# Kernel tuning notes

Hardware: AMD Instinct MI355X
Metric: run time of the kernel (lower is better)

## Reference

```python
import jax, jax.numpy as jnp
import numpy as np

D_MODEL = 1024
NUM_HEADS = 16
DFF = 4096
DEPTH = D_MODEL // NUM_HEADS
EPS = 1e-6


def setup_inputs() -> dict:
    key = jax.random.key(0)
    ks = jax.random.split(key, 12)
    B, S, D = 4, 2048, D_MODEL
    scale = 0.02
    inp = {
        "x": jax.random.normal(ks[0], (B, S, D), dtype=jnp.float32),
        "mask": jnp.zeros((B, 1, 1, S), dtype=jnp.float32),
        "wq": jax.random.normal(ks[1], (D, D), dtype=jnp.float32) * scale,
        "bq": jnp.zeros((D,), dtype=jnp.float32),
        "wk": jax.random.normal(ks[2], (D, D), dtype=jnp.float32) * scale,
        "bk": jnp.zeros((D,), dtype=jnp.float32),
        "wv": jax.random.normal(ks[3], (D, D), dtype=jnp.float32) * scale,
        "bv": jnp.zeros((D,), dtype=jnp.float32),
        "wo": jax.random.normal(ks[4], (D, D), dtype=jnp.float32) * scale,
        "bo": jnp.zeros((D,), dtype=jnp.float32),
        "w1": jax.random.normal(ks[5], (D, DFF), dtype=jnp.float32) * scale,
        "b1": jnp.zeros((DFF,), dtype=jnp.float32),
        "w2": jax.random.normal(ks[6], (DFF, D), dtype=jnp.float32) * scale,
        "b2": jnp.zeros((D,), dtype=jnp.float32),
        "g1": jnp.ones((D,), dtype=jnp.float32),
        "beta1": jnp.zeros((D,), dtype=jnp.float32),
        "g2": jnp.ones((D,), dtype=jnp.float32),
        "beta2": jnp.zeros((D,), dtype=jnp.float32),
    }
    return inp


def _layernorm(x, gamma, beta):
    mu = jnp.mean(x, axis=-1, keepdims=True)
    var = jnp.mean(jnp.square(x - mu), axis=-1, keepdims=True)
    return (x - mu) * jax.lax.rsqrt(var + EPS) * gamma + beta


def _split_heads(t, B, S):
    # [B,S,D] -> [B,H,S,depth]
    return t.reshape(B, S, NUM_HEADS, DEPTH).transpose(0, 2, 1, 3)


def encoder_layer(x, mask, wq, bq, wk, bk, wv, bv, wo, bo,
                  w1, b1, w2, b2, g1, beta1, g2, beta2):
    B, S, D = x.shape
    q = _split_heads(x @ wq + bq, B, S)
    k = _split_heads(x @ wk + bk, B, S)
    v = _split_heads(x @ wv + bv, B, S)
    logits = jnp.einsum("bhqd,bhkd->bhqk", q, k) / jnp.sqrt(
        jnp.asarray(DEPTH, dtype=x.dtype))
    if mask is not None:
        logits = logits + mask * -1e9
    attn = jax.nn.softmax(logits, axis=-1)
    ctx = jnp.einsum("bhqk,bhkd->bhqd", attn, v)
    ctx = ctx.transpose(0, 2, 1, 3).reshape(B, S, D)
    attn_out = ctx @ wo + bo
    out1 = _layernorm(x + attn_out, g1, beta1)
    ffn = jax.nn.relu(out1 @ w1 + b1) @ w2 + b2
    out2 = _layernorm(out1 + ffn, g2, beta2)
    return out2


def reference(x, mask, wq, bq, wk, bk, wv, bv, wo, bo,
              w1, b1, w2, b2, g1, beta1, g2, beta2):
    return encoder_layer(x, mask, wq, bq, wk, bk, wv, bv, wo, bo,
                         w1, b1, w2, b2, g1, beta1, g2, beta2)
```

## Files before the change

kernel.cpp:

```cpp
#include <hip/hip_runtime.h>
#include <cstdint>


#define BATCH 4
#define SEQ   2048
#define DM    1024
#define NH    16
#define DEPTH 64
#define DFF_  4096
#define EPSF  1e-6f

typedef short bf16x8 __attribute__((ext_vector_type(8)));
typedef float f32x4  __attribute__((ext_vector_type(4)));

__device__ __forceinline__ unsigned short f2bf(float f) {
  union { float f; unsigned int u; } v; v.f = f;
  unsigned int u = v.u;
  return (unsigned short)((u + 0x7fffu + ((u >> 16) & 1u)) >> 16);
}

__device__ __forceinline__ void gload_lds16(const void* g, void* l) {
  __builtin_amdgcn_global_load_lds(
      (const __attribute__((address_space(1))) unsigned int*)g,
      (__attribute__((address_space(3))) unsigned int*)l, 16, 0, 0);
}

template<int ACT, int SPLIT, int OUT_BF16>
__global__ __launch_bounds__(256)
void gemm_mfma(const unsigned short* __restrict__ A, const unsigned short* __restrict__ Bt,
               const float* __restrict__ bias, float* __restrict__ Cf,
               unsigned short* __restrict__ Cb, int M, int N, int K)
{
  __shared__ unsigned short As[128 * 32];
  __shared__ unsigned short Bs[128 * 32];
  const int tid  = threadIdx.x;
  const int wid  = tid >> 6;
  const int lane = tid & 63;
  const int wr = wid >> 1, wc = wid & 1;
  const int m0 = blockIdx.y * 128;
  const int n0 = blockIdx.x * 128;

  const int lrow   = lane >> 2;
  const int lchunk = (lane & 3) ^ (lrow & 3);
  const int fr = lane & 15;
  const int kh = lane >> 4;

  f32x4 acc[4][4] = {};

  const char* gA = (const char*)A;
  const char* gB = (const char*)Bt;
  char* lA = (char*)As;
  char* lB = (char*)Bs;

  for (int k0 = 0; k0 < K; k0 += 32) {
#pragma unroll
    for (int seg = 0; seg < 2; ++seg) {
      int r = wid * 32 + seg * 16 + lrow;
      gload_lds16(gA + ((size_t)(m0 + r) * K + k0) * 2 + lchunk * 16,
                  lA + (wid * 32 + seg * 16) * 64);
      gload_lds16(gB + ((size_t)(n0 + r) * K + k0) * 2 + lchunk * 16,
                  lB + (wid * 32 + seg * 16) * 64);
    }
    __syncthreads();
    bf16x8 af[4], bg[4];
#pragma unroll
    for (int i = 0; i < 4; ++i) {
      af[i] = *(const bf16x8*)(lA + (wr * 64 + i * 16 + fr) * 64 + ((kh ^ (fr & 3)) * 16));
      bg[i] = *(const bf16x8*)(lB + (wc * 64 + i * 16 + fr) * 64 + ((kh ^ (fr & 3)) * 16));
    }
#pragma unroll
    for (int i = 0; i < 4; ++i)
#pragma unroll
      for (int j = 0; j < 4; ++j)
        acc[i][j] = __builtin_amdgcn_mfma_f32_16x16x32_bf16(af[i], bg[j], acc[i][j], 0, 0, 0);
    __syncthreads();
  }

  const int rbase = (lane >> 4) * 4;
  const int ccol  = lane & 15;
  float bcol[4];
#pragma unroll
  for (int j = 0; j < 4; ++j) bcol[j] = bias[n0 + wc * 64 + j * 16 + ccol];
#pragma unroll
  for (int i = 0; i < 4; ++i)
#pragma unroll
    for (int jj = 0; jj < 4; ++jj) {
      int row = m0 + wr * 64 + i * 16 + rbase + jj;
#pragma unroll
      for (int j = 0; j < 4; ++j) {
        float vv = acc[i][j][jj] + bcol[j];
        if (ACT) vv = fmaxf(vv, 0.f);
        int col = n0 + wc * 64 + j * 16 + ccol;
        if (SPLIT == 1) {
          int b = row >> 11, s = row & (SEQ - 1);
          int hh = col >> 6, d = col & 63;
          Cb[(((size_t)(b * NH + hh)) * SEQ + s) * DEPTH + d] = f2bf(vv);
        } else if (SPLIT == 2) {
          int b = row >> 11, s = row & (SEQ - 1);
          int hh = col >> 6, d = col & 63;
          Cb[(((size_t)(b * NH + hh)) * DEPTH + d) * SEQ + s] = f2bf(vv);
        } else if (OUT_BF16) {
          Cb[(size_t)row * N + col] = f2bf(vv);
        } else {
          Cf[(size_t)row * N + col] = vv;
        }
      }
    }
}

__global__ __launch_bounds__(256)
void transpose_to_bf16(const float* __restrict__ W, unsigned short* __restrict__ Wt,
                       int K, int N)
{
  __shared__ float t[32][33];
  const int tx = threadIdx.x & 31;
  const int ty = threadIdx.x >> 5;
  const int n0 = blockIdx.x * 32;
  const int k0 = blockIdx.y * 32;
#pragma unroll
  for (int i = 0; i < 4; ++i) {
    int r = ty + i * 8;
    t[r][tx] = W[(size_t)(k0 + r) * N + n0 + tx];
  }
  __syncthreads();
#pragma unroll
  for (int i = 0; i < 4; ++i) {
    int r = ty + i * 8;
    Wt[(size_t)(n0 + r) * K + k0 + tx] = f2bf(t[tx][r]);
  }
}

__global__ __launch_bounds__(256)
void convert_bf16(const float* __restrict__ X, unsigned short* __restrict__ Xb, int n4)
{
  int i = blockIdx.x * 256 + threadIdx.x;
  if (i < n4) {
    float4 v = ((const float4*)X)[i];
    ushort4 r;
    r.x = f2bf(v.x); r.y = f2bf(v.y); r.z = f2bf(v.z); r.w = f2bf(v.w);
    ((ushort4*)Xb)[i] = r;
  }
}

__global__ __launch_bounds__(256)
void attn_mfma(const unsigned short* __restrict__ Qb, const unsigned short* __restrict__ Kb,
               const unsigned short* __restrict__ Vtb, const float* __restrict__ mask,
               unsigned short* __restrict__ ctxb)
{
  __shared__ unsigned short Ks[64 * 64];
  __shared__ unsigned short Vts[64 * 64];
  __shared__ unsigned short Ps[4][16 * 72];
  __shared__ float Ms[SEQ];

  const int tid  = threadIdx.x;
  const int w    = tid >> 6;
  const int lane = tid & 63;
  const int fr   = lane & 15;
  const int kh   = lane >> 4;
  const int rbase = kh * 4;
  const int bh = blockIdx.y;
  const int b  = bh >> 4, hh = bh & 15;
  const int q0 = blockIdx.x * 64;

  for (int i = tid; i < SEQ / 4; i += 256)
    *(float4*)&Ms[i * 4] = *(const float4*)&mask[(size_t)b * SEQ + i * 4];

  const size_t qrow = ((size_t)bh * SEQ + q0 + w * 16 + fr) * DEPTH;
  bf16x8 bq[2];
  bq[0] = *(const bf16x8*)(Qb + qrow + kh * 8);
  bq[1] = *(const bf16x8*)(Qb + qrow + 32 + kh * 8);

  float m_run = -1e30f, l_run = 0.f;
  f32x4 o[4] = {};

  const int stg_chunk = (lane & 7) ^ (lane >> 3);
  const int r8 = lane >> 3;
  unsigned short* Pw = &Ps[w][0];

  for (int kv0 = 0; kv0 < SEQ; kv0 += 64) {
    __syncthreads();
#pragma unroll
    for (int i = 0; i < 2; ++i) {
      int rr = w * 16 + i * 8 + r8;
      gload_lds16((const char*)Kb + (((size_t)bh * SEQ + kv0 + rr) * DEPTH) * 2 + stg_chunk * 16,
                  (char*)Ks + (w * 16 + i * 8) * 128);
      gload_lds16((const char*)Vtb + (((size_t)bh * DEPTH + rr) * SEQ + kv0) * 2 + stg_chunk * 16,
                  (char*)Vts + (w * 16 + i * 8) * 128);
    }
    __syncthreads();

    f32x4 s[4] = {};
#pragma unroll
    for (int ks = 0; ks < 2; ++ks)
#pragma unroll
      for (int j = 0; j < 4; ++j) {
        bf16x8 ak = *(const bf16x8*)((const char*)Ks + (j * 16 + fr) * 128 +
                                     (((ks * 4 + kh) ^ (fr & 7)) * 16));
        s[j] = __builtin_amdgcn_mfma_f32_16x16x32_bf16(ak, bq[ks], s[j], 0, 0, 0);
      }

    float p[16];
    float pmax = -1e30f;
#pragma unroll
    for (int j = 0; j < 4; ++j) {
      float4 mk = *(const float4*)&Ms[kv0 + j * 16 + rbase];
#pragma unroll
      for (int jj = 0; jj < 4; ++jj) {
        float vsc = s[j][jj] * 0.125f + ((const float*)&mk)[jj] * (-1e9f);
        p[j * 4 + jj] = vsc;
        pmax = fmaxf(pmax, vsc);
      }
    }
    pmax = fmaxf(pmax, __shfl_xor(pmax, 16));
    pmax = fmaxf(pmax, __shfl_xor(pmax, 32));
    float mnew = fmaxf(m_run, pmax);
    float sc = __expf(m_run - mnew);
    float rs = 0.f;
#pragma unroll
    for (int t = 0; t < 16; ++t) { p[t] = __expf(p[t] - mnew); rs += p[t]; }
    rs += __shfl_xor(rs, 16);
    rs += __shfl_xor(rs, 32);
    l_run = l_run * sc + rs;
    m_run = mnew;
#pragma unroll
    for (int db = 0; db < 4; ++db) {
      o[db][0] *= sc; o[db][1] *= sc; o[db][2] *= sc; o[db][3] *= sc;
    }

#pragma unroll
    for (int j = 0; j < 4; ++j) {
      unsigned int lo = (unsigned)f2bf(p[j * 4 + 0]) | ((unsigned)f2bf(p[j * 4 + 1]) << 16);
      unsigned int hi = (unsigned)f2bf(p[j * 4 + 2]) | ((unsigned)f2bf(p[j * 4 + 3]) << 16);
      unsigned long long pk = (unsigned long long)lo | ((unsigned long long)hi << 32);
      *(unsigned long long*)((char*)Pw + fr * 144 + (j * 16 + rbase) * 2) = pk;
    }
#pragma unroll
    for (int ks = 0; ks < 2; ++ks) {
      bf16x8 bp = *(const bf16x8*)((char*)Pw + fr * 144 + ks * 64 + kh * 16);
#pragma unroll
      for (int db = 0; db < 4; ++db) {
        bf16x8 av = *(const bf16x8*)((const char*)Vts + (db * 16 + fr) * 128 +
                                     (((ks * 4 + kh) ^ (fr & 7)) * 16));
        o[db] = __builtin_amdgcn_mfma_f32_16x16x32_bf16(av, bp, o[db], 0, 0, 0);
      }
    }
  }

  float inv = 1.f / l_run;
  const int srow = q0 + w * 16 + fr;
#pragma unroll
  for (int db = 0; db < 4; ++db) {
    ushort4 rb;
    rb.x = f2bf(o[db][0] * inv); rb.y = f2bf(o[db][1] * inv);
    rb.z = f2bf(o[db][2] * inv); rb.w = f2bf(o[db][3] * inv);
    *(ushort4*)(ctxb + ((size_t)(b * SEQ + srow)) * DM + hh * 64 + db * 16 + rbase) = rb;
  }
}

template<int DUAL>
__global__ __launch_bounds__(256)
void add_ln_kernel(const float* __restrict__ X, const float* __restrict__ Y,
                   const float* __restrict__ g, const float* __restrict__ be,
                   float* __restrict__ out, unsigned short* __restrict__ outb)
{
  __shared__ float red[8];
  const int row = blockIdx.x;
  const int tid = threadIdx.x;
  const size_t off = (size_t)row * DM + tid * 4;
  float4 xv = *(const float4*)(X + off);
  float4 yv = *(const float4*)(Y + off);
  float v0 = xv.x + yv.x, v1 = xv.y + yv.y, v2 = xv.z + yv.z, v3 = xv.w + yv.w;
  float s = v0 + v1 + v2 + v3;
#pragma unroll
  for (int m = 1; m < 64; m <<= 1) s += __shfl_xor(s, m);
  if ((tid & 63) == 0) red[tid >> 6] = s;
  __syncthreads();
  float mean = (red[0] + red[1] + red[2] + red[3]) * (1.f / DM);
  float d0 = v0 - mean, d1 = v1 - mean, d2 = v2 - mean, d3 = v3 - mean;
  float sq = d0 * d0 + d1 * d1 + d2 * d2 + d3 * d3;
#pragma unroll
  for (int m = 1; m < 64; m <<= 1) sq += __shfl_xor(sq, m);
  if ((tid & 63) == 0) red[4 + (tid >> 6)] = sq;
  __syncthreads();
  float var = (red[4] + red[5] + red[6] + red[7]) * (1.f / DM);
  float inv = rsqrtf(var + EPSF);
  int col = tid * 4;
  float4 r;
  r.x = d0 * inv * g[col + 0] + be[col + 0];
  r.y = d1 * inv * g[col + 1] + be[col + 1];
  r.z = d2 * inv * g[col + 2] + be[col + 2];
  r.w = d3 * inv * g[col + 3] + be[col + 3];
  *(float4*)(out + off) = r;
  if (DUAL) {
    ushort4 rb;
    rb.x = f2bf(r.x); rb.y = f2bf(r.y); rb.z = f2bf(r.z); rb.w = f2bf(r.w);
    *(ushort4*)(outb + off) = rb;
  }
}

extern "C" void kernel_launch(void* const* d_in, const int* in_sizes, int n_in,
                              void* d_out, int out_size, void* d_ws, size_t ws_size,
                              hipStream_t stream)
{
  const float* x    = (const float*)d_in[0];
  const float* mask = (const float*)d_in[1];
  const float* wq   = (const float*)d_in[2];
  const float* bq   = (const float*)d_in[3];
  const float* wk   = (const float*)d_in[4];
  const float* bk   = (const float*)d_in[5];
  const float* wv   = (const float*)d_in[6];
  const float* bv   = (const float*)d_in[7];
  const float* wo   = (const float*)d_in[8];
  const float* bo   = (const float*)d_in[9];
  const float* w1   = (const float*)d_in[10];
  const float* b1   = (const float*)d_in[11];
  const float* w2   = (const float*)d_in[12];
  const float* b2   = (const float*)d_in[13];
  const float* g1   = (const float*)d_in[14];
  const float* be1  = (const float*)d_in[15];
  const float* g2   = (const float*)d_in[16];
  const float* be2  = (const float*)d_in[17];
  float* out = (float*)d_out;
  char* wsb = (char*)d_ws;

  unsigned short* qb   = (unsigned short*)(wsb);
  unsigned short* kb   = (unsigned short*)(wsb + (16u << 20));
  unsigned short* vtb  = (unsigned short*)(wsb + (32u << 20));
  unsigned short* ctxb = (unsigned short*)(wsb + (48u << 20));
  unsigned short* xb   = (unsigned short*)(wsb + (64u << 20));
  unsigned short* hbuf = (unsigned short*)(wsb + (80u << 20));
  unsigned short* wqt  = (unsigned short*)(wsb + (112u << 20));
  unsigned short* wkt  = (unsigned short*)(wsb + (114u << 20));
  unsigned short* wvt  = (unsigned short*)(wsb + (116u << 20));
  unsigned short* wot  = (unsigned short*)(wsb + (118u << 20));
  unsigned short* w1t  = (unsigned short*)(wsb + (120u << 20));
  unsigned short* w2t  = (unsigned short*)(wsb + (128u << 20));
  float* attn_out = (float*)(wsb);
  float* out1     = (float*)(wsb + (32u << 20));
  unsigned short* out1b = xb;
  float* ffn      = (float*)(wsb);

  dim3 blk(256);

  convert_bf16<<<8192, blk, 0, stream>>>(x, xb, (BATCH * SEQ * DM) / 4);
  transpose_to_bf16<<<dim3(32, 32), blk, 0, stream>>>(wq, wqt, DM, DM);
  transpose_to_bf16<<<dim3(32, 32), blk, 0, stream>>>(wk, wkt, DM, DM);
  transpose_to_bf16<<<dim3(32, 32), blk, 0, stream>>>(wv, wvt, DM, DM);
  transpose_to_bf16<<<dim3(32, 32), blk, 0, stream>>>(wo, wot, DM, DM);
  transpose_to_bf16<<<dim3(128, 32), blk, 0, stream>>>(w1, w1t, DM, DFF_);
  transpose_to_bf16<<<dim3(32, 128), blk, 0, stream>>>(w2, w2t, DFF_, DM);

  const int M = BATCH * SEQ;
  gemm_mfma<0, 1, 0><<<dim3(8, 64), blk, 0, stream>>>(xb, wqt, bq, nullptr, qb, M, DM, DM);
  gemm_mfma<0, 1, 0><<<dim3(8, 64), blk, 0, stream>>>(xb, wkt, bk, nullptr, kb, M, DM, DM);
  gemm_mfma<0, 2, 0><<<dim3(8, 64), blk, 0, stream>>>(xb, wvt, bv, nullptr, vtb, M, DM, DM);

  attn_mfma<<<dim3(SEQ / 64, BATCH * NH), blk, 0, stream>>>(qb, kb, vtb, mask, ctxb);

  gemm_mfma<0, 0, 0><<<dim3(8, 64), blk, 0, stream>>>(ctxb, wot, bo, attn_out, nullptr, M, DM, DM);
  add_ln_kernel<1><<<dim3(M), blk, 0, stream>>>(x, attn_out, g1, be1, out1, out1b);

  for (int c = 0; c < 2; ++c) {
    gemm_mfma<1, 0, 1><<<dim3(32, 32), blk, 0, stream>>>(
        out1b + (size_t)c * 4096 * DM, w1t, b1, nullptr, hbuf, 4096, DFF_, DM);
    gemm_mfma<0, 0, 0><<<dim3(8, 32), blk, 0, stream>>>(
        hbuf, w2t, b2, ffn + (size_t)c * 4096 * DM, nullptr, 4096, DM, DFF_);
  }
  add_ln_kernel<0><<<dim3(M), blk, 0, stream>>>(out1, ffn, g2, be2, out, nullptr);
}
```

Baseline: 767.1 us.

## Replace GEMM with 256x256 double-buffered 8-wave kernel and fuse QKV projections

Replaces the 128x128 single-buffered GEMM with a 512-thread kernel using 256x256 output tiles. It uses a 64-wide K step, double-buffered 128KB LDS loaded asynchronously with manual vmcnt waits, and s_setprio around the MFMA bursts. Workgroups are swizzled across the flattened grid for cache locality. The Q/K/V weights are concatenated so one N=3072 GEMM writes all three head-split outputs. The FFN now runs as two full-M GEMMs instead of two chunks. The aims are more data reuse per tile, overlap of global loads with MFMA work, and fewer launches, at the cost of lower occupancy and hand-tuned wait counts that could be fragile.

```diff
diff --git a/kernel.cpp b/kernel.cpp
--- a/kernel.cpp
+++ b/kernel.cpp
@@ -25,87 +25,183 @@
       (__attribute__((address_space(3))) unsigned int*)l, 16, 0, 0);
 }
 
-template<int ACT, int SPLIT, int OUT_BF16>
-__global__ __launch_bounds__(256)
-void gemm_mfma(const unsigned short* __restrict__ A, const unsigned short* __restrict__ Bt,
-               const float* __restrict__ bias, float* __restrict__ Cf,
-               unsigned short* __restrict__ Cb, int M, int N, int K)
-{
-  __shared__ unsigned short As[128 * 32];
-  __shared__ unsigned short Bs[128 * 32];
+#define VMCNT(n) asm volatile("s_waitcnt vmcnt(" #n ")" ::: "memory")
+
+template<int EPI>
+__global__ __launch_bounds__(512, 2)
+void gemm8(const unsigned short* __restrict__ A, const unsigned short* __restrict__ Bt,
+           const float* __restrict__ bias0, const float* __restrict__ bias1,
+           const float* __restrict__ bias2, float* __restrict__ Cf,
+           unsigned short* __restrict__ Cb0, unsigned short* __restrict__ Cb1,
+           unsigned short* __restrict__ Cb2, int M, int N, int K)
+{
+  __shared__ char smem[131072];
   const int tid  = threadIdx.x;
+  const int lane = tid & 63;
   const int wid  = tid >> 6;
-  const int lane = tid & 63;
-  const int wr = wid >> 1, wc = wid & 1;
-  const int m0 = blockIdx.y * 128;
-  const int n0 = blockIdx.x * 128;
-
-  const int lrow   = lane >> 2;
-  const int lchunk = (lane & 3) ^ (lrow & 3);
-  const int fr = lane & 15;
-  const int kh = lane >> 4;
-
-  f32x4 acc[4][4] = {};
-
-  const char* gA = (const char*)A;
-  const char* gB = (const char*)Bt;
-  char* lA = (char*)As;
-  char* lB = (char*)Bs;
-
-  for (int k0 = 0; k0 < K; k0 += 32) {
-#pragma unroll
-    for (int seg = 0; seg < 2; ++seg) {
-      int r = wid * 32 + seg * 16 + lrow;
-      gload_lds16(gA + ((size_t)(m0 + r) * K + k0) * 2 + lchunk * 16,
-                  lA + (wid * 32 + seg * 16) * 64);
-      gload_lds16(gB + ((size_t)(n0 + r) * K + k0) * 2 + lchunk * 16,
-                  lB + (wid * 32 + seg * 16) * 64);
-    }
-    __syncthreads();
-    bf16x8 af[4], bg[4];
-#pragma unroll
-    for (int i = 0; i < 4; ++i) {
-      af[i] = *(const bf16x8*)(lA + (wr * 64 + i * 16 + fr) * 64 + ((kh ^ (fr & 3)) * 16));
-      bg[i] = *(const bf16x8*)(lB + (wc * 64 + i * 16 + fr) * 64 + ((kh ^ (fr & 3)) * 16));
-    }
-#pragma unroll
-    for (int i = 0; i < 4; ++i)
-#pragma unroll
-      for (int j = 0; j < 4; ++j)
-        acc[i][j] = __builtin_amdgcn_mfma_f32_16x16x32_bf16(af[i], bg[j], acc[i][j], 0, 0, 0);
-    __syncthreads();
-  }
-
-  const int rbase = (lane >> 4) * 4;
-  const int ccol  = lane & 15;
-  float bcol[4];
-#pragma unroll
-  for (int j = 0; j < 4; ++j) bcol[j] = bias[n0 + wc * 64 + j * 16 + ccol];
-#pragma unroll
-  for (int i = 0; i < 4; ++i)
-#pragma unroll
-    for (int jj = 0; jj < 4; ++jj) {
-      int row = m0 + wr * 64 + i * 16 + rbase + jj;
+  const int wr   = wid >> 2;
+  const int wcn  = wid & 3;
+  const int fr   = lane & 15;
+  const int kh   = lane >> 4;
+
+  const int nbx  = N >> 8;
+  const int nwg  = gridDim.x;
+  const int flat = blockIdx.x;
+  const int swz  = (flat & 7) * (nwg >> 3) + (flat >> 3);
+  const int bx = swz % nbx, by = swz / nbx;
+  const int m0 = by << 8, n0 = bx << 8;
+
+  const int lr  = tid >> 3;
+  const int ch  = tid & 7;
+  const int sch = ch ^ (lr & 7);
+  const char* gA = (const char*)A + ((size_t)(m0 + lr) * K) * 2 + sch * 16;
+  const char* gB = (const char*)Bt + ((size_t)(n0 + lr) * K) * 2 + sch * 16;
+  const size_t rstep = (size_t)K * 128;
+
+  const int chk0 = ((kh) ^ (fr & 7)) * 16;
+  const int chk1 = ((4 + kh) ^ (fr & 7)) * 16;
+  const int rowA = wr * 128 + fr;
+  const int rowB = wcn * 64 + fr;
+
+  f32x4 acc[8][4] = {};
+  bf16x8 bg[4][2];
+  const int NT = K >> 6;
+
+  {
+    char* sb = smem;
+    gload_lds16(gB + 0 * rstep, sb + 32768 + 0 * 8192 + tid * 16);
+    gload_lds16(gB + 1 * rstep, sb + 32768 + 1 * 8192 + tid * 16);
+    gload_lds16(gB + 2 * rstep, sb + 32768 + 2 * 8192 + tid * 16);
+    gload_lds16(gB + 3 * rstep, sb + 32768 + 3 * 8192 + tid * 16);
+    gload_lds16(gA + 0 * rstep, sb + 0 * 8192 + tid * 16);
+    gload_lds16(gA + 2 * rstep, sb + 2 * 8192 + tid * 16);
+    gload_lds16(gA + 1 * rstep, sb + 1 * 8192 + tid * 16);
+    gload_lds16(gA + 3 * rstep, sb + 3 * 8192 + tid * 16);
+    VMCNT(2);
+    __builtin_amdgcn_s_barrier();
+  }
+
+  for (int t = 0; t < NT - 1; ++t) {
+    char* rb = smem + ((t & 1) << 16);
+    char* sb = smem + (((t + 1) & 1) << 16);
+    const size_t kg = (size_t)(t + 1) * 128;
+#pragma unroll
+    for (int p = 0; p < 4; ++p) {
+      if (p == 0) {
+        gload_lds16(gB + kg + 0 * rstep, sb + 32768 + 0 * 8192 + tid * 16);
+        gload_lds16(gB + kg + 1 * rstep, sb + 32768 + 1 * 8192 + tid * 16);
+      } else if (p == 1) {
+        gload_lds16(gB + kg + 2 * rstep, sb + 32768 + 2 * 8192 + tid * 16);
+        gload_lds16(gB + kg + 3 * rstep, sb + 32768 + 3 * 8192 + tid * 16);
+      } else if (p == 2) {
+        gload_lds16(gA + kg + 0 * rstep, sb + 0 * 8192 + tid * 16);
+        gload_lds16(gA + kg + 2 * rstep, sb + 2 * 8192 + tid * 16);
+      } else {
+        gload_lds16(gA + kg + 1 * rstep, sb + 1 * 8192 + tid * 16);
+        gload_lds16(gA + kg + 3 * rstep, sb + 3 * 8192 + tid * 16);
+      }
+      if (p == 0) {
+#pragma unroll
+        for (int j = 0; j < 4; ++j) {
+          bg[j][0] = *(const bf16x8*)(rb + 32768 + (rowB + j * 16) * 128 + chk0);
+          bg[j][1] = *(const bf16x8*)(rb + 32768 + (rowB + j * 16) * 128 + chk1);
+        }
+      }
+      bf16x8 a00 = *(const bf16x8*)(rb + (rowA + (2 * p) * 16) * 128 + chk0);
+      bf16x8 a01 = *(const bf16x8*)(rb + (rowA + (2 * p) * 16) * 128 + chk1);
+      bf16x8 a10 = *(const bf16x8*)(rb + (rowA + (2 * p + 1) * 16) * 128 + chk0);
+      bf16x8 a11 = *(const bf16x8*)(rb + (rowA + (2 * p + 1) * 16) * 128 + chk1);
+      __builtin_amdgcn_s_barrier();
+      __builtin_amdgcn_s_setprio(1);
 #pragma unroll
       for (int j = 0; j < 4; ++j) {
-        float vv = acc[i][j][jj] + bcol[j];
-        if (ACT) vv = fmaxf(vv, 0.f);
-        int col = n0 + wc * 64 + j * 16 + ccol;
-        if (SPLIT == 1) {
-          int b = row >> 11, s = row & (SEQ - 1);
-          int hh = col >> 6, d = col & 63;
-          Cb[(((size_t)(b * NH + hh)) * SEQ + s) * DEPTH + d] = f2bf(vv);
-        } else if (SPLIT == 2) {
-          int b = row >> 11, s = row & (SEQ - 1);
-          int hh = col >> 6, d = col & 63;
-          Cb[(((size_t)(b * NH + hh)) * DEPTH + d) * SEQ + s] = f2bf(vv);
-        } else if (OUT_BF16) {
-          Cb[(size_t)row * N + col] = f2bf(vv);
-        } else {
-          Cf[(size_t)row * N + col] = vv;
+        acc[2*p][j]   = __builtin_amdgcn_mfma_f32_16x16x32_bf16(a00, bg[j][0], acc[2*p][j], 0, 0, 0);
+        acc[2*p][j]   = __builtin_amdgcn_mfma_f32_16x16x32_bf16(a01, bg[j][1], acc[2*p][j], 0, 0, 0);
+        acc[2*p+1][j] = __builtin_amdgcn_mfma_f32_16x16x32_bf16(a10, bg[j][0], acc[2*p+1][j], 0, 0, 0);
+        acc[2*p+1][j] = __builtin_amdgcn_mfma_f32_16x16x32_bf16(a11, bg[j][1], acc[2*p+1][j], 0, 0, 0);
+      }
+      __builtin_amdgcn_s_setprio(0);
+      if (p == 1) VMCNT(4);
+      if (p == 3) VMCNT(2);
+      __builtin_amdgcn_s_barrier();
+    }
+  }
+  {
+    char* rb = smem + (((NT - 1) & 1) << 16);
+#pragma unroll
+    for (int p = 0; p < 4; ++p) {
+      if (p == 0) {
+#pragma unroll
+        for (int j = 0; j < 4; ++j) {
+          bg[j][0] = *(const bf16x8*)(rb + 32768 + (rowB + j * 16) * 128 + chk0);
+          bg[j][1] = *(const bf16x8*)(rb + 32768 + (rowB + j * 16) * 128 + chk1);
         }
       }
-    }
+      bf16x8 a00 = *(const bf16x8*)(rb + (rowA + (2 * p) * 16) * 128 + chk0);
+      bf16x8 a01 = *(const bf16x8*)(rb + (rowA + (2 * p) * 16) * 128 + chk1);
+      bf16x8 a10 = *(const bf16x8*)(rb + (rowA + (2 * p + 1) * 16) * 128 + chk0);
+      bf16x8 a11 = *(const bf16x8*)(rb + (rowA + (2 * p + 1) * 16) * 128 + chk1);
+      __builtin_amdgcn_s_barrier();
+      __builtin_amdgcn_s_setprio(1);
+#pragma unroll
+      for (int j = 0; j < 4; ++j) {
+        acc[2*p][j]   = __builtin_amdgcn_mfma_f32_16x16x32_bf16(a00, bg[j][0], acc[2*p][j], 0, 0, 0);
+        acc[2*p][j]   = __builtin_amdgcn_mfma_f32_16x16x32_bf16(a01, bg[j][1], acc[2*p][j], 0, 0, 0);
+        acc[2*p+1][j] = __builtin_amdgcn_mfma_f32_16x16x32_bf16(a10, bg[j][0], acc[2*p+1][j], 0, 0, 0);
+        acc[2*p+1][j] = __builtin_amdgcn_mfma_f32_16x16x32_bf16(a11, bg[j][1], acc[2*p+1][j], 0, 0, 0);
+      }
+      __builtin_amdgcn_s_setprio(0);
+      if (p == 1) VMCNT(0);
+      __builtin_amdgcn_s_barrier();
+    }
+  }
+
+  if (EPI == 2) {
+    const int seg = n0 >> 10;
+    const float* bp = seg == 0 ? bias0 : (seg == 1 ? bias1 : bias2);
+    unsigned short* dst = seg == 0 ? Cb0 : (seg == 1 ? Cb1 : Cb2);
+    float bc[4];
+#pragma unroll
+    for (int j = 0; j < 4; ++j) bc[j] = bp[(n0 & 1023) + wcn * 64 + j * 16 + fr];
+#pragma unroll
+    for (int m = 0; m < 8; ++m)
+#pragma unroll
+      for (int jj = 0; jj < 4; ++jj) {
+        const int row = m0 + wr * 128 + m * 16 + kh * 4 + jj;
+        const int b = row >> 11, s = row & (SEQ - 1);
+#pragma unroll
+        for (int j = 0; j < 4; ++j) {
+          const int cs = (n0 & 1023) + wcn * 64 + j * 16 + fr;
+          const int hh = cs >> 6, d = cs & 63;
+          const float v = acc[m][j][jj] + bc[j];
+          if (seg < 2)
+            dst[(((size_t)(b * NH + hh)) * SEQ + s) * DEPTH + d] = f2bf(v);
+          else
+            dst[(((size_t)(b * NH + hh)) * DEPTH + d) * SEQ + s] = f2bf(v);
+        }
+      }
+  } else {
+    float bc[4];
+#pragma unroll
+    for (int j = 0; j < 4; ++j) bc[j] = bias0[n0 + wcn * 64 + j * 16 + fr];
+#pragma unroll
+    for (int m = 0; m < 8; ++m)
+#pragma unroll
+      for (int jj = 0; jj < 4; ++jj) {
+        const int row = m0 + wr * 128 + m * 16 + kh * 4 + jj;
+#pragma unroll
+        for (int j = 0; j < 4; ++j) {
+          const int col = n0 + wcn * 64 + j * 16 + fr;
+          float v = acc[m][j][jj] + bc[j];
+          if (EPI == 1) {
+            v = fmaxf(v, 0.f);
+            Cb0[(size_t)row * N + col] = f2bf(v);
+          } else {
+            Cf[(size_t)row * N + col] = v;
+          }
+        }
+      }
+  }
 }
 
 __global__ __launch_bounds__(256)
@@ -323,48 +419,45 @@
   float* out = (float*)d_out;
   char* wsb = (char*)d_ws;
 
-  unsigned short* qb   = (unsigned short*)(wsb);
-  unsigned short* kb   = (unsigned short*)(wsb + (16u << 20));
-  unsigned short* vtb  = (unsigned short*)(wsb + (32u << 20));
-  unsigned short* ctxb = (unsigned short*)(wsb + (48u << 20));
-  unsigned short* xb   = (unsigned short*)(wsb + (64u << 20));
-  unsigned short* hbuf = (unsigned short*)(wsb + (80u << 20));
-  unsigned short* wqt  = (unsigned short*)(wsb + (112u << 20));
-  unsigned short* wkt  = (unsigned short*)(wsb + (114u << 20));
-  unsigned short* wvt  = (unsigned short*)(wsb + (116u << 20));
-  unsigned short* wot  = (unsigned short*)(wsb + (118u << 20));
-  unsigned short* w1t  = (unsigned short*)(wsb + (120u << 20));
-  unsigned short* w2t  = (unsigned short*)(wsb + (128u << 20));
+  unsigned short* qb    = (unsigned short*)(wsb);
+  unsigned short* kb    = (unsigned short*)(wsb + (16u << 20));
+  unsigned short* vtb   = (unsigned short*)(wsb + (32u << 20));
+  unsigned short* ctxb  = (unsigned short*)(wsb + (48u << 20));
+  unsigned short* xb    = (unsigned short*)(wsb + (64u << 20));
+  unsigned short* hbuf  = (unsigned short*)(wsb + (80u << 20));
+  unsigned short* wqkvt = (unsigned short*)(wsb + (144u << 20));
+  unsigned short* wot   = (unsigned short*)(wsb + (150u << 20));
+  unsigned short* w1t   = (unsigned short*)(wsb + (152u << 20));
+  unsigned short* w2t   = (unsigned short*)(wsb + (160u << 20));
   float* attn_out = (float*)(wsb);
   float* out1     = (float*)(wsb + (32u << 20));
   unsigned short* out1b = xb;
   float* ffn      = (float*)(wsb);
 
   dim3 blk(256);
+  const int M = BATCH * SEQ;
 
   convert_bf16<<<8192, blk, 0, stream>>>(x, xb, (BATCH * SEQ * DM) / 4);
-  transpose_to_bf16<<<dim3(32, 32), blk, 0, stream>>>(wq, wqt, DM, DM);
-  transpose_to_bf16<<<dim3(32, 32), blk, 0, stream>>>(wk, wkt, DM, DM);
-  transpose_to_bf16<<<dim3(32, 32), blk, 0, stream>>>(wv, wvt, DM, DM);
+  transpose_to_bf16<<<dim3(32, 32), blk, 0, stream>>>(wq, wqkvt, DM, DM);
+  transpose_to_bf16<<<dim3(32, 32), blk, 0, stream>>>(wk, wqkvt + 1024 * 1024, DM, DM);
+  transpose_to_bf16<<<dim3(32, 32), blk, 0, stream>>>(wv, wqkvt + 2 * 1024 * 1024, DM, DM);
   transpose_to_bf16<<<dim3(32, 32), blk, 0, stream>>>(wo, wot, DM, DM);
   transpose_to_bf16<<<dim3(128, 32), blk, 0, stream>>>(w1, w1t, DM, DFF_);
   transpose_to_bf16<<<dim3(32, 128), blk, 0, stream>>>(w2, w2t, DFF_, DM);
 
-  const int M = BATCH * SEQ;
-  gemm_mfma<0, 1, 0><<<dim3(8, 64), blk, 0, stream>>>(xb, wqt, bq, nullptr, qb, M, DM, DM);
-  gemm_mfma<0, 1, 0><<<dim3(8, 64), blk, 0, stream>>>(xb, wkt, bk, nullptr, kb, M, DM, DM);
-  gemm_mfma<0, 2, 0><<<dim3(8, 64), blk, 0, stream>>>(xb, wvt, bv, nullptr, vtb, M, DM, DM);
+  gemm8<2><<<dim3((M / 256) * (3072 / 256)), dim3(512), 0, stream>>>(
+      xb, wqkvt, bq, bk, bv, nullptr, qb, kb, vtb, M, 3072, DM);
 
   attn_mfma<<<dim3(SEQ / 64, BATCH * NH), blk, 0, stream>>>(qb, kb, vtb, mask, ctxb);
 
-  gemm_mfma<0, 0, 0><<<dim3(8, 64), blk, 0, stream>>>(ctxb, wot, bo, attn_out, nullptr, M, DM, DM);
+  gemm8<0><<<dim3((M / 256) * (DM / 256)), dim3(512), 0, stream>>>(
+      ctxb, wot, bo, nullptr, nullptr, attn_out, nullptr, nullptr, nullptr, M, DM, DM);
   add_ln_kernel<1><<<dim3(M), blk, 0, stream>>>(x, attn_out, g1, be1, out1, out1b);
 
-  for (int c = 0; c < 2; ++c) {
-    gemm_mfma<1, 0, 1><<<dim3(32, 32), blk, 0, stream>>>(
-        out1b + (size_t)c * 4096 * DM, w1t, b1, nullptr, hbuf, 4096, DFF_, DM);
-    gemm_mfma<0, 0, 0><<<dim3(8, 32), blk, 0, stream>>>(
-        hbuf, w2t, b2, ffn + (size_t)c * 4096 * DM, nullptr, 4096, DM, DFF_);
-  }
+  gemm8<1><<<dim3((M / 256) * (DFF_ / 256)), dim3(512), 0, stream>>>(
+      out1b, w1t, b1, nullptr, nullptr, nullptr, hbuf, nullptr, nullptr, M, DFF_, DM);
+  gemm8<0><<<dim3((M / 256) * (DM / 256)), dim3(512), 0, stream>>>(
+      hbuf, w2t, b2, nullptr, nullptr, ffn, nullptr, nullptr, nullptr, M, DM, DFF_);
+
   add_ln_kernel<0><<<dim3(M), blk, 0, stream>>>(out1, ffn, g2, be2, out, nullptr);
 }
```

Result: faster. 636.4 us (-17.0%).
